# Kernel optimization log

Measured on AMD Instinct MI355X. Metric: run time of the kernel, lower is better.

The kernel has to match this reference:

```python
import jax, jax.numpy as jnp
import numpy as np
from jax import lax


def conv3d(x, w, b):
    # x: (B,W,D,H,Cin), w: (kW,kD,kH,Cin,Cout), 'same' padding, stride 1
    return lax.conv_general_dilated(
        x, w, window_strides=(1, 1, 1), padding='SAME',
        dimension_numbers=('NDHWC', 'DHWIO', 'NDHWC')) + b


def proj(x, w, b, s, o):
    # Conv3D -> BatchNorm (inference, folded to per-channel affine) -> ReLU
    return jax.nn.relu(conv3d(x, w, b) * s + o)


def setup_inputs() -> dict:
    key = jax.random.key(0)
    ks = jax.random.split(key, 6)
    B, W, D, H, C = 2, 16, 16, 16, 32
    WS = 0.05  # weight scale to keep sigmoid of the NxN chain unsaturated
    return {
        'x': jax.random.normal(ks[0], (B, W, D, H, C), jnp.float32),
        'gamma': jax.random.uniform(ks[1], (1,), jnp.float32),
        'q_w': jax.random.normal(ks[2], (1, 3, 1, C, 8), jnp.float32) * WS,
        'q_b': jnp.zeros((8,), jnp.float32),
        'q_s': jnp.ones((8,), jnp.float32),
        'q_o': jnp.zeros((8,), jnp.float32),
        'k_w': jax.random.normal(ks[3], (3, 1, 1, C, 8), jnp.float32) * WS,
        'k_b': jnp.zeros((8,), jnp.float32),
        'k_s': jnp.ones((8,), jnp.float32),
        'k_o': jnp.zeros((8,), jnp.float32),
        'j_w': jax.random.normal(ks[4], (1, 1, 3, C, 8), jnp.float32) * WS,
        'j_b': jnp.zeros((8,), jnp.float32),
        'j_s': jnp.ones((8,), jnp.float32),
        'j_o': jnp.zeros((8,), jnp.float32),
        'v_w': jax.random.normal(ks[5], (1, 1, 1, C, C), jnp.float32) * WS,
        'v_b': jnp.zeros((C,), jnp.float32),
        'v_s': jnp.ones((C,), jnp.float32),
        'v_o': jnp.zeros((C,), jnp.float32),
    }


def reference(x, gamma, q_w, q_b, q_s, q_o, k_w, k_b, k_s, k_o,
              j_w, j_b, j_s, j_o, v_w, v_b, v_s, v_o):
    B, W, D, H, C = x.shape
    N = W * D * H
    # Q/K/J: (B,W,D,H,8) -> row-major reshape to (B,8,N) exactly as tf Reshape
    Qt = jnp.swapaxes(proj(x, q_w, q_b, q_s, q_o).reshape(B, -1, N), 1, 2)  # (B,N,8)
    K = proj(x, k_w, k_b, k_s, k_o).reshape(B, -1, N)                        # (B,8,N)
    Jt = jnp.swapaxes(proj(x, j_w, j_b, j_s, j_o).reshape(B, -1, N), 1, 2)  # (B,N,8)
    V = proj(x, v_w, v_b, v_s, v_o).reshape(B, N, -1)                        # (B,N,C)
    m1 = jnp.matmul(Qt, K)          # (B,N,N)
    m2 = jnp.matmul(Jt, K)          # (B,N,N)
    affinity = jax.nn.sigmoid(jnp.matmul(m1, m2))  # (B,N,N)
    weights = jnp.matmul(affinity, V).reshape(B, W, D, H, C)
    return gamma * weights + x
```

## Files before the change

kernel.cpp:

```cpp
#include <hip/hip_runtime.h>
#include <cstddef>

#define NN 4096
#define JSPLIT 8

typedef short bf16x8 __attribute__((ext_vector_type(8)));
typedef float f32x4 __attribute__((ext_vector_type(4)));

__device__ __forceinline__ unsigned short f2bf(float f) {
    union { float f; unsigned u; } v; v.f = f;
    unsigned r = v.u + 0x7fffu + ((v.u >> 16) & 1u);
    return (unsigned short)(r >> 16);
}

__global__ __launch_bounds__(256) void kA(
    const float* __restrict__ x,
    const float* __restrict__ qw, const float* __restrict__ qb,
    const float* __restrict__ qs, const float* __restrict__ qo,
    const float* __restrict__ kw, const float* __restrict__ kb,
    const float* __restrict__ ks, const float* __restrict__ ko,
    const float* __restrict__ jw, const float* __restrict__ jb,
    const float* __restrict__ js, const float* __restrict__ jo,
    const float* __restrict__ vw, const float* __restrict__ vb,
    const float* __restrict__ vs, const float* __restrict__ vo,
    float* __restrict__ Qf, float* __restrict__ Kf,
    unsigned short* __restrict__ Vt, float* __restrict__ Mm)
{
    __shared__ float vw_s[1024];
    __shared__ float cw_s[3 * 776];
    __shared__ float Kl[32][8];
    __shared__ float Jl[32][8];
    const int t = threadIdx.x;
    for (int i = t; i < 1024; i += 256) vw_s[i] = vw[i];
    for (int i = t; i < 768; i += 256) {
        cw_s[i]        = qw[i];
        cw_s[776 + i]  = kw[i];
        cw_s[1552 + i] = jw[i];
    }
    __syncthreads();

    const int spi = t >> 3;
    const int gsp = blockIdx.x * 32 + spi;
    const int b   = gsp >> 12;
    const int sp  = gsp & 4095;
    const int w = sp >> 8, d = (sp >> 4) & 15, h = sp & 15;
    const float4* xr = (const float4*)(x + (size_t)gsp * 32);

    {
        const int c4 = t & 7;
        float4 acc = make_float4(0.f, 0.f, 0.f, 0.f);
        #pragma unroll
        for (int c8 = 0; c8 < 8; ++c8) {
            const float4 xv = xr[c8];
            #pragma unroll
            for (int k = 0; k < 4; ++k) {
                const float xs = (k == 0) ? xv.x : (k == 1) ? xv.y : (k == 2) ? xv.z : xv.w;
                const float4 wv = *(const float4*)&vw_s[(c8 * 4 + k) * 32 + c4 * 4];
                acc.x += xs * wv.x; acc.y += xs * wv.y;
                acc.z += xs * wv.z; acc.w += xs * wv.w;
            }
        }
        const float4 bb = ((const float4*)vb)[c4];
        const float4 sc = ((const float4*)vs)[c4];
        const float4 oo = ((const float4*)vo)[c4];
        float4 r;
        r.x = fmaxf((acc.x + bb.x) * sc.x + oo.x, 0.f);
        r.y = fmaxf((acc.y + bb.y) * sc.y + oo.y, 0.f);
        r.z = fmaxf((acc.z + bb.z) * sc.z + oo.z, 0.f);
        r.w = fmaxf((acc.w + bb.w) * sc.w + oo.w, 0.f);
        unsigned short* vt = Vt + (size_t)b * 131072 + (size_t)(c4 * 4) * 4096 + sp;
        vt[0]        = f2bf(r.x);
        vt[4096]     = f2bf(r.y);
        vt[2 * 4096] = f2bf(r.z);
        vt[3 * 4096] = f2bf(r.w);
    }

    {
        const int g = t & 7;
        if (g < 6) {
            const int conv = g >> 1;
            const int co4  = g & 1;
            const int coord  = (conv == 0) ? d : (conv == 1) ? w : h;
            const int stride = (conv == 0) ? 16 : (conv == 1) ? 256 : 1;
            const float* cw = cw_s + conv * 776;
            float4 acc = make_float4(0.f, 0.f, 0.f, 0.f);
            #pragma unroll
            for (int tap = 0; tap < 3; ++tap) {
                const int cc = coord + tap - 1;
                if (cc < 0 || cc > 15) continue;
                const float4* xt = (const float4*)(x + (size_t)(gsp + (tap - 1) * stride) * 32);
                #pragma unroll
                for (int c8 = 0; c8 < 8; ++c8) {
                    const float4 xv = xt[c8];
                    #pragma unroll
                    for (int k = 0; k < 4; ++k) {
                        const float xs = (k == 0) ? xv.x : (k == 1) ? xv.y : (k == 2) ? xv.z : xv.w;
                        const float4 wv = *(const float4*)&cw[tap * 256 + (c8 * 4 + k) * 8 + co4 * 4];
                        acc.x += xs * wv.x; acc.y += xs * wv.y;
                        acc.z += xs * wv.z; acc.w += xs * wv.w;
                    }
                }
            }
            const float* bbp = (conv == 0) ? qb : (conv == 1) ? kb : jb;
            const float* scp = (conv == 0) ? qs : (conv == 1) ? ks : js;
            const float* oop = (conv == 0) ? qo : (conv == 1) ? ko : jo;
            const float4 bb = ((const float4*)bbp)[co4];
            const float4 sc = ((const float4*)scp)[co4];
            const float4 oo = ((const float4*)oop)[co4];
            float4 r;
            r.x = fmaxf((acc.x + bb.x) * sc.x + oo.x, 0.f);
            r.y = fmaxf((acc.y + bb.y) * sc.y + oo.y, 0.f);
            r.z = fmaxf((acc.z + bb.z) * sc.z + oo.z, 0.f);
            r.w = fmaxf((acc.w + bb.w) * sc.w + oo.w, 0.f);
            if (conv == 0) {
                ((float4*)(Qf + (size_t)b * 32768 + (size_t)sp * 8))[co4] = r;
            } else if (conv == 1) {
                ((float4*)(Kf + (size_t)b * 32768 + (size_t)sp * 8))[co4] = r;
                *(float4*)&Kl[spi][co4 * 4] = r;
            } else {
                *(float4*)&Jl[spi][co4 * 4] = r;
            }
        }
    }

    __syncthreads();
    if (t < 64) {
        const int r = t >> 3, s = t & 7;
        float acc = 0.f;
        #pragma unroll 8
        for (int i = 0; i < 32; ++i) acc += Kl[i][r] * Jl[i][s];
        atomicAdd(&Mm[b * 64 + t], acc);
    }
}

__global__ __launch_bounds__(256) void kD(
    const float* __restrict__ Qf, const float* __restrict__ Mm,
    const float* __restrict__ Kf, const unsigned short* __restrict__ Vt,
    const float* __restrict__ gamma, float* __restrict__ out)
{
    const int blk = blockIdx.x;
    const int jsp = blk & 7;
    const int rt  = (blk >> 3) & 63;
    const int b   = blk >> 9;
    const int i0  = rt * 64;
    const int j0  = jsp * 512;
    const int t   = threadIdx.x;
    const int jg = t & 15, rg = t >> 4;
    const int w = t >> 6, lane = t & 63;
    const int m = lane & 15, quad = lane >> 4;

    __shared__ float m_s[64];
    __shared__ float kt_s[8][68];
    __shared__ unsigned short s_lds[64][72];

    if (t < 64) m_s[t] = Mm[b * 64 + t];
    __syncthreads();

    float P[4][8];
    {
        float a[4][8];
        #pragma unroll
        for (int r = 0; r < 8; ++r) {
            const float* qr = Qf + (size_t)b * 32768 + (size_t)r * 4096 + i0 + rg * 4;
            #pragma unroll
            for (int ri = 0; ri < 4; ++ri) a[ri][r] = qr[ri];
        }
        #pragma unroll
        for (int s = 0; s < 8; ++s) {
            #pragma unroll
            for (int ri = 0; ri < 4; ++ri) {
                float acc = 0.f;
                #pragma unroll
                for (int r = 0; r < 8; ++r) acc += a[ri][r] * m_s[r * 8 + s];
                P[ri][s] = acc;
            }
        }
    }

    const float* Kb = Kf + (size_t)b * 32768;
    const unsigned short* Vb = Vt + (size_t)b * 131072;

    f32x4 acc0 = {0.f, 0.f, 0.f, 0.f};
    f32x4 acc1 = {0.f, 0.f, 0.f, 0.f};

    for (int jc = 0; jc < 8; ++jc) {
        const int jb = j0 + jc * 64;
        __syncthreads();
        if (t < 128) {
            const int rr = t >> 4, j4 = (t & 15) * 4;
            *(float4*)&kt_s[rr][j4] = *(const float4*)(Kb + (size_t)rr * 4096 + jb + j4);
        }
        __syncthreads();
        float sv[4][4];
        #pragma unroll
        for (int jt = 0; jt < 4; ++jt) {
            const int j = jg * 4 + jt;
            float kv[8];
            #pragma unroll
            for (int r = 0; r < 8; ++r) kv[r] = kt_s[r][j];
            #pragma unroll
            for (int ri = 0; ri < 4; ++ri) {
                float dsum = 0.f;
                #pragma unroll
                for (int r = 0; r < 8; ++r) dsum += P[ri][r] * kv[r];
                sv[ri][jt] = __builtin_amdgcn_rcpf(1.0f + __expf(-dsum));
            }
        }
        #pragma unroll
        for (int ri = 0; ri < 4; ++ri) {
            const unsigned p01 = (unsigned)f2bf(sv[ri][0]) | ((unsigned)f2bf(sv[ri][1]) << 16);
            const unsigned p23 = (unsigned)f2bf(sv[ri][2]) | ((unsigned)f2bf(sv[ri][3]) << 16);
            *(uint2*)&s_lds[rg * 4 + ri][jg * 4] = make_uint2(p01, p23);
        }
        __syncthreads();
        #pragma unroll
        for (int kt = 0; kt < 2; ++kt) {
            const bf16x8 af = *(const bf16x8*)&s_lds[w * 16 + m][kt * 32 + quad * 8];
            {
                const bf16x8 bv = *(const bf16x8*)(Vb + (size_t)m * 4096 + jb + kt * 32 + quad * 8);
                acc0 = __builtin_amdgcn_mfma_f32_16x16x32_bf16(af, bv, acc0, 0, 0, 0);
            }
            {
                const bf16x8 bv = *(const bf16x8*)(Vb + (size_t)(16 + m) * 4096 + jb + kt * 32 + quad * 8);
                acc1 = __builtin_amdgcn_mfma_f32_16x16x32_bf16(af, bv, acc1, 0, 0, 0);
            }
        }
    }

    const float g = gamma[0];
    #pragma unroll
    for (int reg = 0; reg < 4; ++reg) {
        const int row = i0 + w * 16 + quad * 4 + reg;
        float* op = out + ((size_t)b * 4096 + row) * 32 + m;
        atomicAdd(op,      g * acc0[reg]);
        atomicAdd(op + 16, g * acc1[reg]);
    }
}

extern "C" void kernel_launch(void* const* d_in, const int* in_sizes, int n_in,
                              void* d_out, int out_size, void* d_ws, size_t ws_size,
                              hipStream_t stream)
{
    const float* x     = (const float*)d_in[0];
    const float* gamma = (const float*)d_in[1];
    const float* qw = (const float*)d_in[2];
    const float* qb = (const float*)d_in[3];
    const float* qs = (const float*)d_in[4];
    const float* qo = (const float*)d_in[5];
    const float* kw = (const float*)d_in[6];
    const float* kb = (const float*)d_in[7];
    const float* ks = (const float*)d_in[8];
    const float* ko = (const float*)d_in[9];
    const float* jw = (const float*)d_in[10];
    const float* jb = (const float*)d_in[11];
    const float* js = (const float*)d_in[12];
    const float* jo = (const float*)d_in[13];
    const float* vw = (const float*)d_in[14];
    const float* vb = (const float*)d_in[15];
    const float* vs = (const float*)d_in[16];
    const float* vo = (const float*)d_in[17];

    float* ws = (float*)d_ws;
    float* Qf = ws;
    float* Kf = ws + 65536;
    float* Mm = ws + 131072;
    unsigned short* Vt = (unsigned short*)(ws + 131200);

    hipMemsetAsync(Mm, 0, 128 * sizeof(float), stream);
    hipMemcpyAsync(d_out, x, (size_t)262144 * sizeof(float),
                   hipMemcpyDeviceToDevice, stream);
    kA<<<256, 256, 0, stream>>>(x, qw, qb, qs, qo, kw, kb, ks, ko,
                                jw, jb, js, jo, vw, vb, vs, vo,
                                Qf, Kf, Vt, Mm);
    kD<<<1024, 256, 0, stream>>>(Qf, Mm, Kf, Vt, gamma, (float*)d_out);
}
```

Measured before the change: 131.0 us.

## Preload K slice once, double-buffer sigmoid tile, and use packed FMA/exp2 sigmoid

The K slice for the whole 512-column chunk is loaded into LDS once up front instead of per 64-column step. The sigmoid tile buffer is double-buffered so each iteration needs only one barrier, and V fragments are prefetched at the top of the loop. The score computation uses packed two-wide FMAs with log2e folded into P, raw v_exp_f32, and hardware packed bf16 conversion, and the MFMA section runs at raised wave priority. The larger LDS footprint may reduce occupancy, and the hardware conversion rounding may differ slightly from the manual round-to-nearest.

```diff
diff --git a/kernel.cpp b/kernel.cpp
--- a/kernel.cpp
+++ b/kernel.cpp
@@ -2,10 +2,10 @@
 #include <cstddef>
 
 #define NN 4096
-#define JSPLIT 8
 
 typedef short bf16x8 __attribute__((ext_vector_type(8)));
 typedef float f32x4 __attribute__((ext_vector_type(4)));
+typedef float f32x2 __attribute__((ext_vector_type(2)));
 
 __device__ __forceinline__ unsigned short f2bf(float f) {
     union { float f; unsigned u; } v; v.f = f;
@@ -150,13 +150,22 @@
     const int m = lane & 15, quad = lane >> 4;
 
     __shared__ float m_s[64];
-    __shared__ float kt_s[8][68];
-    __shared__ unsigned short s_lds[64][72];
+    __shared__ float kt_s[8][516];
+    __shared__ unsigned short s_lds[2][64][72];
+
+    const float* Kb = Kf + (size_t)b * 32768;
+    const unsigned short* Vb = Vt + (size_t)b * 131072;
 
     if (t < 64) m_s[t] = Mm[b * 64 + t];
+    #pragma unroll
+    for (int v = 0; v < 4; ++v) {
+        const int idx = t + v * 256;
+        const int r = idx >> 7, j4 = (idx & 127) << 2;
+        *(float4*)&kt_s[r][j4] = *(const float4*)(Kb + (size_t)r * 4096 + j0 + j4);
+    }
     __syncthreads();
 
-    float P[4][8];
+    float P2[4][8];
     {
         float a[4][8];
         #pragma unroll
@@ -172,59 +181,64 @@
                 float acc = 0.f;
                 #pragma unroll
                 for (int r = 0; r < 8; ++r) acc += a[ri][r] * m_s[r * 8 + s];
-                P[ri][s] = acc;
-            }
-        }
-    }
-
-    const float* Kb = Kf + (size_t)b * 32768;
-    const unsigned short* Vb = Vt + (size_t)b * 131072;
+                P2[ri][s] = acc * -1.44269504f;
+            }
+        }
+    }
 
     f32x4 acc0 = {0.f, 0.f, 0.f, 0.f};
     f32x4 acc1 = {0.f, 0.f, 0.f, 0.f};
 
+    #pragma unroll 1
     for (int jc = 0; jc < 8; ++jc) {
         const int jb = j0 + jc * 64;
+        const bf16x8 bv00 = *(const bf16x8*)(Vb + (size_t)m * 4096 + jb + quad * 8);
+        const bf16x8 bv10 = *(const bf16x8*)(Vb + (size_t)m * 4096 + jb + 32 + quad * 8);
+        const bf16x8 bv01 = *(const bf16x8*)(Vb + (size_t)(16 + m) * 4096 + jb + quad * 8);
+        const bf16x8 bv11 = *(const bf16x8*)(Vb + (size_t)(16 + m) * 4096 + jb + 32 + quad * 8);
+
+        unsigned short (*sl)[72] = s_lds[jc & 1];
+
+        unsigned hpk[4][2];
+        #pragma unroll
+        for (int tp = 0; tp < 2; ++tp) {
+            const int jcol = jg * 4 + tp * 2;
+            f32x2 pa[4];
+            #pragma unroll
+            for (int ri = 0; ri < 4; ++ri) pa[ri] = (f32x2){0.f, 0.f};
+            #pragma unroll
+            for (int r = 0; r < 8; ++r) {
+                const f32x2 kv = *(const f32x2*)&kt_s[r][jcol];
+                #pragma unroll
+                for (int ri = 0; ri < 4; ++ri)
+                    pa[ri] = __builtin_elementwise_fma((f32x2){P2[ri][r], P2[ri][r]}, kv, pa[ri]);
+            }
+            #pragma unroll
+            for (int ri = 0; ri < 4; ++ri) {
+                float e0, e1;
+                asm("v_exp_f32 %0, %1" : "=v"(e0) : "v"(pa[ri].x));
+                asm("v_exp_f32 %0, %1" : "=v"(e1) : "v"(pa[ri].y));
+                const float s0 = __builtin_amdgcn_rcpf(1.0f + e0);
+                const float s1 = __builtin_amdgcn_rcpf(1.0f + e1);
+                unsigned pk;
+                asm("v_cvt_pk_bf16_f32 %0, %1, %2" : "=v"(pk) : "v"(s0), "v"(s1));
+                hpk[ri][tp] = pk;
+            }
+        }
+        #pragma unroll
+        for (int ri = 0; ri < 4; ++ri)
+            *(uint2*)&sl[rg * 4 + ri][jg * 4] = make_uint2(hpk[ri][0], hpk[ri][1]);
+
         __syncthreads();
-        if (t < 128) {
-            const int rr = t >> 4, j4 = (t & 15) * 4;
-            *(float4*)&kt_s[rr][j4] = *(const float4*)(Kb + (size_t)rr * 4096 + jb + j4);
-        }
-        __syncthreads();
-        float sv[4][4];
-        #pragma unroll
-        for (int jt = 0; jt < 4; ++jt) {
-            const int j = jg * 4 + jt;
-            float kv[8];
-            #pragma unroll
-            for (int r = 0; r < 8; ++r) kv[r] = kt_s[r][j];
-            #pragma unroll
-            for (int ri = 0; ri < 4; ++ri) {
-                float dsum = 0.f;
-                #pragma unroll
-                for (int r = 0; r < 8; ++r) dsum += P[ri][r] * kv[r];
-                sv[ri][jt] = __builtin_amdgcn_rcpf(1.0f + __expf(-dsum));
-            }
-        }
-        #pragma unroll
-        for (int ri = 0; ri < 4; ++ri) {
-            const unsigned p01 = (unsigned)f2bf(sv[ri][0]) | ((unsigned)f2bf(sv[ri][1]) << 16);
-            const unsigned p23 = (unsigned)f2bf(sv[ri][2]) | ((unsigned)f2bf(sv[ri][3]) << 16);
-            *(uint2*)&s_lds[rg * 4 + ri][jg * 4] = make_uint2(p01, p23);
-        }
-        __syncthreads();
-        #pragma unroll
-        for (int kt = 0; kt < 2; ++kt) {
-            const bf16x8 af = *(const bf16x8*)&s_lds[w * 16 + m][kt * 32 + quad * 8];
-            {
-                const bf16x8 bv = *(const bf16x8*)(Vb + (size_t)m * 4096 + jb + kt * 32 + quad * 8);
-                acc0 = __builtin_amdgcn_mfma_f32_16x16x32_bf16(af, bv, acc0, 0, 0, 0);
-            }
-            {
-                const bf16x8 bv = *(const bf16x8*)(Vb + (size_t)(16 + m) * 4096 + jb + kt * 32 + quad * 8);
-                acc1 = __builtin_amdgcn_mfma_f32_16x16x32_bf16(af, bv, acc1, 0, 0, 0);
-            }
-        }
+
+        __builtin_amdgcn_s_setprio(1);
+        const bf16x8 af0 = *(const bf16x8*)&sl[w * 16 + m][quad * 8];
+        const bf16x8 af1 = *(const bf16x8*)&sl[w * 16 + m][32 + quad * 8];
+        acc0 = __builtin_amdgcn_mfma_f32_16x16x32_bf16(af0, bv00, acc0, 0, 0, 0);
+        acc1 = __builtin_amdgcn_mfma_f32_16x16x32_bf16(af0, bv01, acc1, 0, 0, 0);
+        acc0 = __builtin_amdgcn_mfma_f32_16x16x32_bf16(af1, bv10, acc0, 0, 0, 0);
+        acc1 = __builtin_amdgcn_mfma_f32_16x16x32_bf16(af1, bv11, acc1, 0, 0, 0);
+        __builtin_amdgcn_s_setprio(0);
     }
 
     const float g = gamma[0];
```

New measurement: 121.6 us. -7.2%, faster.
